# Performance work log

Hardware: AMD Instinct MI355X
Metric: run time of the kernel (lower is better)

## Reference

```python
import jax, jax.numpy as jnp
import numpy as np
from jax import lax

K = 5          # CARAFE kernel_size
S = 2          # scale_factor (downsample stride)
GROUP = 1      # mask groups
ENC_PAD = 1    # (encoder_kernel-1)*dilation//2 with encoder_kernel=3


def _conv2d(x, w, b, stride, padding, dilation=1):
    y = lax.conv_general_dilated(
        x, w, window_strides=(stride, stride),
        padding=[(padding, padding), (padding, padding)],
        rhs_dilation=(dilation, dilation),
        dimension_numbers=('NCHW', 'OIHW', 'NCHW'))
    return y + b[None, :, None, None]


def setup_inputs() -> dict:
    key = jax.random.key(0)
    k1, k2, k3 = jax.random.split(key, 3)
    B, C, H, W = 4, 256, 128, 128
    COMP = 64
    x = jax.random.normal(k1, (B, C, H, W), dtype=jnp.float32)
    # xavier-uniform-ish scale for compressor, std=0.001 for content encoder (as in init_weights)
    w1 = jax.random.normal(k2, (COMP, C, 1, 1), dtype=jnp.float32) * (1.0 / np.sqrt(C))
    b1 = jnp.zeros((COMP,), dtype=jnp.float32)
    w2 = jax.random.normal(k3, (K * K * GROUP, COMP, 3, 3), dtype=jnp.float32) * 0.001
    b2 = jnp.zeros((K * K * GROUP,), dtype=jnp.float32)
    return {"x": x, "w1": w1, "b1": b1, "w2": w2, "b2": b2}


def _carafe_forward(x, w1, b1, w2, b2):
    B, C, H, W = x.shape
    compressed = _conv2d(x, w1, b1, stride=1, padding=0)           # (B, 64, H, W)
    mask = _conv2d(compressed, w2, b2, stride=S, padding=ENC_PAD)   # (B, K*K*G, Ho, Wo)
    Ho, Wo = mask.shape[2], mask.shape[3]
    # kernel_normalizer: softmax over the K*K window per group
    mask = jax.nn.softmax(mask.reshape(B, GROUP, K * K, Ho, Wo), axis=2)
    # feature_reassemble: fused unfold * mask sum — accumulate per kernel tap to
    # avoid materializing the full (B, C, K*K, Ho, Wo) tensor.
    pad = K // 2
    x_pad = jnp.pad(x, ((0, 0), (0, 0), (pad, pad), (pad, pad)))
    Cg = C // GROUP
    out = jnp.zeros((B, GROUP, Cg, Ho, Wo), dtype=x.dtype)
    for i in range(K):
        for j in range(K):
            patch = x_pad[:, :, i:i + S * (Ho - 1) + 1:S, j:j + S * (Wo - 1) + 1:S]
            patch = patch.reshape(B, GROUP, Cg, Ho, Wo)
            out = out + patch * mask[:, :, i * K + j][:, :, None]
    return out.reshape(B, C, Ho, Wo)


def reference(x, w1, b1, w2, b2):
    return _carafe_forward(x, w1, b1, w2, b2)
```

## Files before the change

kernel.cpp:

```cpp
#include <hip/hip_runtime.h>
#include <math.h>

#define BN   4
#define CN   256
#define HN   128
#define WN   128
#define COMP 64
#define KK   25
#define HO   64
#define WO   64

#define W1B_OFF  0
#define W2A_OFF  8192
#define MASK_OFF 17408
#define COMP_OFF 427008
#define WS_NEED  ((size_t)(COMP_OFF + (size_t)BN * HN * WN * COMP / 2) * 4)

typedef short v8s  __attribute__((ext_vector_type(8)));
typedef float v16f __attribute__((ext_vector_type(16)));

__device__ inline ushort f2bf(float f) {
  unsigned u = __float_as_uint(f);
  return (ushort)((u + 0x7fffu + ((u >> 16) & 1u)) >> 16);
}

__global__ __launch_bounds__(64) void compose_frags(
    const float* __restrict__ w1, const float* __restrict__ w2,
    float* __restrict__ ws) {
  const int bid = blockIdx.x;
  const int lane = threadIdx.x;
  const int k0 = (lane >> 5) * 8;
  ushort pk[8];
  ushort* dst;
  if (bid < 32) {
    const int kidx = bid >> 1, nt = bid & 1;
    const int ch = nt * 32 + (lane & 31);
    const int c0 = kidx * 16 + k0;
#pragma unroll
    for (int j = 0; j < 8; ++j) pk[j] = f2bf(w1[(size_t)ch * CN + c0 + j]);
    dst = (ushort*)(ws + W1B_OFF) + ((size_t)((kidx * 2 + nt) * 64 + lane)) * 8;
  } else {
    const int g = bid - 32;
    const int t = g >> 2, kidx = g & 3;
    const int m = lane & 31;
    const int kk0 = kidx * 16 + k0;
#pragma unroll
    for (int j = 0; j < 8; ++j) {
      float v = (m < KK) ? w2[((size_t)(m * COMP + kk0 + j)) * 9 + t] : 0.f;
      pk[j] = f2bf(v);
    }
    dst = (ushort*)(ws + W2A_OFF) + ((size_t)((t * 4 + kidx) * 64 + lane)) * 8;
  }
  *(ushort4*)(dst)     = make_ushort4(pk[0], pk[1], pk[2], pk[3]);
  *(ushort4*)(dst + 4) = make_ushort4(pk[4], pk[5], pk[6], pk[7]);
}

__global__ __launch_bounds__(256, 4) void compress_kernel(
    const float* __restrict__ x, const float* __restrict__ b1,
    float* __restrict__ ws) {
  const int h = blockIdx.x, b = blockIdx.y;
  const int tid = threadIdx.x;
  const int lane = tid & 63, w = tid >> 6;
  const int nn = lane & 31, kh = lane >> 5;
  const int px = w * 32 + nn;
  const ushort* w1B = (const ushort*)(ws + W1B_OFF);
  v16f acc[2] = {{}, {}};
#pragma unroll 2
  for (int kidx = 0; kidx < 16; ++kidx) {
    const float* xc = x + (((size_t)(b * CN + kidx * 16 + kh * 8)) * HN + h) * WN + px;
    float av[8];
#pragma unroll
    for (int j = 0; j < 8; ++j) av[j] = xc[(size_t)j * (HN * WN)];
    v8s af;
#pragma unroll
    for (int j = 0; j < 8; ++j) af[j] = (short)f2bf(av[j]);
    v8s bf0 = *(const v8s*)(w1B + ((size_t)((kidx * 2 + 0) * 64 + lane)) * 8);
    v8s bf1 = *(const v8s*)(w1B + ((size_t)((kidx * 2 + 1) * 64 + lane)) * 8);
    acc[0] = __builtin_amdgcn_mfma_f32_32x32x16_bf16(af, bf0, acc[0], 0, 0, 0);
    acc[1] = __builtin_amdgcn_mfma_f32_32x32x16_bf16(af, bf1, acc[1], 0, 0, 0);
  }
  ushort* comp = (ushort*)(ws + COMP_OFF);
  const size_t rowbase = (size_t)(b * HN + h) * WN;
#pragma unroll
  for (int nt = 0; nt < 2; ++nt) {
    const float bias = b1[nt * 32 + nn];
#pragma unroll
    for (int rg = 0; rg < 16; ++rg) {
      const int pr = w * 32 + (rg & 3) + 8 * (rg >> 2) + 4 * kh;
      comp[(rowbase + pr) * COMP + nt * 32 + nn] = f2bf(acc[nt][rg] + bias);
    }
  }
}

#define MS_LDS 49152
__global__ __launch_bounds__(256, 4) void mask_softmax(
    const float* __restrict__ b2, float* __restrict__ ws) {
  const int ho = blockIdx.x, b = blockIdx.y;
  const int tid = threadIdx.x;
  const int lane = tid & 63, w = tid >> 6;
  __shared__ __attribute__((aligned(16))) char smem[MS_LDS];
  float* red = (float*)smem;
  const ushort* comp = (const ushort*)(ws + COMP_OFF);

#pragma unroll
  for (int i = 0; i < 12; ++i) {
    const int flat = i * 256 + tid;
    const int r = flat >> 10;
    const int px = (flat >> 3) & 127;
    const int cg = flat & 7;
    const int rr = 2 * ho + r - 1;
    v8s v = {};
    if (rr >= 0)
      v = *(const v8s*)(comp + ((size_t)(b * HN + rr) * WN + px) * COMP + cg * 8);
    const int boff = (((r * 128 + px) * 64 + cg * 8) * 2) ^ (((px >> 1) & 7) << 4);
    *(v8s*)(smem + boff) = v;
  }
  __syncthreads();

  const int nt = w & 1, kh2 = w >> 1;
  const int nn = lane & 31;
  const ushort* w2A = (const ushort*)(ws + W2A_OFF);
  const v8s zero8 = {};
  v16f acc = {};
#pragma unroll
  for (int t = 0; t < 9; ++t) {
    const int dr = t / 3, dc = t % 3;
#pragma unroll
    for (int ki = 0; ki < 2; ++ki) {
      const int kidx = kh2 * 2 + ki;
      const v8s af = *(const v8s*)(w2A + ((size_t)((t * 4 + kidx) * 64 + lane)) * 8);
      const int q = 2 * (nt * 32 + nn) + dc - 1;
      const bool bad = q < 0;
      const int qc = bad ? 0 : q;
      const int boff = (((dr * 128 + qc) * 64 + kidx * 16 + (lane >> 5) * 8) * 2)
                       ^ (((qc >> 1) & 7) << 4);
      v8s bf = *(const v8s*)(smem + boff);
      if (dc == 0 && bad) bf = zero8;
      acc = __builtin_amdgcn_mfma_f32_32x32x16_bf16(af, bf, acc, 0, 0, 0);
    }
  }
  __syncthreads();

  if (kh2 == 1) {
#pragma unroll
    for (int rg = 0; rg < 16; ++rg) {
      const int m = (rg & 3) + 8 * (rg >> 2) + 4 * (lane >> 5);
      if (m < KK) red[(nt * KK + m) * 32 + nn] = acc[rg];
    }
  }
  __syncthreads();
  if (kh2 == 0) {
#pragma unroll
    for (int rg = 0; rg < 16; ++rg) {
      const int m = (rg & 3) + 8 * (rg >> 2) + 4 * (lane >> 5);
      if (m < KK) red[(nt * KK + m) * 32 + nn] += acc[rg];
    }
  }
  __syncthreads();

  if (tid < 64) {
    const int wo = tid;
    const int tnt = wo >> 5, tc = wo & 31;
    float logit[KK];
    float mx = -1e30f;
#pragma unroll
    for (int m = 0; m < KK; ++m) {
      float l = b2[m] + red[(tnt * KK + m) * 32 + tc];
      logit[m] = l;
      mx = fmaxf(mx, l);
    }
    float ssum = 0.f;
#pragma unroll
    for (int m = 0; m < KK; ++m) {
      float e = __expf(logit[m] - mx);
      logit[m] = e;
      ssum += e;
    }
    const float inv = 1.f / ssum;
    float* mdst = ws + MASK_OFF + (size_t)(b * HO + ho) * KK * 64;
#pragma unroll
    for (int m = 0; m < KK; ++m) mdst[m * 64 + wo] = logit[m] * inv;
  }
}

__global__ __launch_bounds__(256, 4) void gather_kernel(
    const float* __restrict__ ws, const float* __restrict__ x,
    float* __restrict__ out) {
  const int bid0 = blockIdx.x;
  const int bid = (bid0 & 7) * 128 + (bid0 >> 3);
  const int ho = bid & 63;
  const int cq = (bid >> 6) & 3;
  const int b = bid >> 8;
  const int tid = threadIdx.x;
  const int lane = tid & 63, wv = tid >> 6;

  __shared__ float sml[KK * 64];

  const float* __restrict__ xb = x + (size_t)(b * CN) * (HN * WN);
  const int wo = lane;
  const int c_base = __builtin_amdgcn_readfirstlane(cq * 64 + wv * 16);
  const int col = 2 * wo;
  float2 g[2][5];
  auto load_g = [&](int ci, float2* dst) {
    const float* xc = xb + (size_t)(c_base + ci) * (HN * WN);
#pragma unroll
    for (int i = 0; i < 5; ++i) {
      int r = 2 * ho - 2 + i;
      dst[i] = (r >= 0 && r < HN) ? *(const float2*)(xc + r * WN + col)
                                  : make_float2(0.f, 0.f);
    }
  };
  load_g(0, g[0]);
  load_g(1, g[1]);

  const float* msrc = ws + MASK_OFF + (size_t)(b * HO + ho) * KK * 64;
  for (int i = tid; i < KK * 64; i += 256) sml[i] = msrc[i];
  __syncthreads();

  float smr[KK];
#pragma unroll
  for (int m = 0; m < KK; ++m) smr[m] = sml[m * 64 + wo];

  const float wok = (wo > 0) ? 1.f : 0.f;
  const float w63 = (wo < 63) ? 1.f : 0.f;
  for (int ci = 0; ci < 16; ++ci) {
    float2 v[5];
#pragma unroll
    for (int i = 0; i < 5; ++i) v[i] = g[ci & 1][i];
    if (ci + 2 < 16) load_g(ci + 2, g[ci & 1]);

    float acc2 = 0.f;
#pragma unroll
    for (int i = 0; i < 5; ++i) {
      float lx = wok * __shfl_up(v[i].x, 1, 64);
      float ly = wok * __shfl_up(v[i].y, 1, 64);
      float rx = w63 * __shfl_down(v[i].x, 1, 64);
      acc2 += lx * smr[i * 5 + 0] + ly * smr[i * 5 + 1]
            + v[i].x * smr[i * 5 + 2] + v[i].y * smr[i * 5 + 3]
            + rx * smr[i * 5 + 4];
    }
    out[(((size_t)(b * CN + c_base + ci)) * HO + ho) * WO + wo] = acc2;
  }
}

#define FB_WSTRIDE 240
#define FB_TB_OFF  (256 * FB_WSTRIDE)

__global__ __launch_bounds__(256) void compose_w_fb(
    const float* __restrict__ w1, const float* __restrict__ b1,
    const float* __restrict__ w2, float* __restrict__ ws) {
  int mt = blockIdx.x, c = threadIdx.x;
  float acc = 0.f;
#pragma unroll 8
  for (int k = 0; k < COMP; ++k)
    acc += w2[(size_t)(mt / 9 * COMP + k) * 9 + (mt % 9)] * w1[k * CN + c];
  ws[c * FB_WSTRIDE + mt] = acc;
  if (mt < FB_WSTRIDE - 225) ws[c * FB_WSTRIDE + 225 + mt] = 0.f;
  if (c == 0) {
    float tbv = 0.f;
    for (int k = 0; k < COMP; ++k)
      tbv += w2[(size_t)(mt / 9 * COMP + k) * 9 + (mt % 9)] * b1[k];
    ws[FB_TB_OFF + mt] = tbv;
  }
}

__global__ __launch_bounds__(1024, 4) void fused_fb(
    const float* __restrict__ x, const float* __restrict__ b2,
    const float* __restrict__ ws, float* __restrict__ out) {
  const int ho = blockIdx.x, b = blockIdx.y, tid = threadIdx.x;
  const int wo = tid & 63, wv = tid >> 6;
  const int c_base = __builtin_amdgcn_readfirstlane(wv * 16);
  const float* __restrict__ w2c = ws;
  const float* __restrict__ tb  = ws + FB_TB_OFF;
  __shared__ float red[8 * KK * 64];
  __shared__ float sm[KK * 64];
  const float* __restrict__ xb = x + (size_t)(b * CN) * (HN * WN);
  const int col = 2 * wo;
  float acc[KK];
#pragma unroll
  for (int m = 0; m < KK; ++m) acc[m] = 0.f;
  float2 xbuf[2][3];
  auto load_ch = [&](int ci, float2* dst) {
    const float* xc = xb + (size_t)(c_base + ci) * (HN * WN);
    dst[0] = (ho > 0) ? *(const float2*)(xc + (2 * ho - 1) * WN + col)
                      : make_float2(0.f, 0.f);
    dst[1] = *(const float2*)(xc + (2 * ho) * WN + col);
    dst[2] = *(const float2*)(xc + (2 * ho + 1) * WN + col);
  };
  load_ch(0, xbuf[0]);
  load_ch(1, xbuf[1]);
  const float wok = (wo > 0) ? 1.f : 0.f;
  for (int ci = 0; ci < 16; ++ci) {
    float2 r0 = xbuf[ci & 1][0], r1 = xbuf[ci & 1][1], r2 = xbuf[ci & 1][2];
    if (ci + 2 < 16) load_ch(ci + 2, xbuf[ci & 1]);
    float xv[9];
    xv[0] = wok * __shfl_up(r0.y, 1, 64); xv[1] = r0.x; xv[2] = r0.y;
    xv[3] = wok * __shfl_up(r1.y, 1, 64); xv[4] = r1.x; xv[5] = r1.y;
    xv[6] = wok * __shfl_up(r2.y, 1, 64); xv[7] = r2.x; xv[8] = r2.y;
    const float* __restrict__ wrow = w2c + (size_t)(c_base + ci) * FB_WSTRIDE;
#pragma unroll
    for (int m = 0; m < KK; ++m) {
      float a = acc[m];
#pragma unroll
      for (int t = 0; t < 9; ++t) a += wrow[m * 9 + t] * xv[t];
      acc[m] = a;
    }
  }
  float2 g[2][5];
  auto load_g = [&](int ci, float2* dst) {
    const float* xc = xb + (size_t)(c_base + ci) * (HN * WN);
#pragma unroll
    for (int i = 0; i < 5; ++i) {
      int r = 2 * ho - 2 + i;
      dst[i] = (r >= 0 && r < HN) ? *(const float2*)(xc + r * WN + col)
                                  : make_float2(0.f, 0.f);
    }
  };
  load_g(0, g[0]);
  load_g(1, g[1]);
  if (wv >= 8) {
#pragma unroll
    for (int m = 0; m < KK; ++m) red[((wv - 8) * KK + m) * 64 + wo] = acc[m];
  }
  __syncthreads();
  if (wv < 8) {
#pragma unroll
    for (int m = 0; m < KK; ++m) red[(wv * KK + m) * 64 + wo] += acc[m];
  }
  __syncthreads();
  if (wv < 4) {
#pragma unroll
    for (int m = 0; m < KK; ++m)
      red[(wv * KK + m) * 64 + wo] += red[((wv + 4) * KK + m) * 64 + wo];
  }
  __syncthreads();
  if (wv < 2) {
#pragma unroll
    for (int m = 0; m < KK; ++m)
      red[(wv * KK + m) * 64 + wo] += red[((wv + 2) * KK + m) * 64 + wo];
  }
  __syncthreads();
  if (tid < 64) {
    const float vr0 = (ho > 0) ? 1.f : 0.f;
    const float vq0 = (wo > 0) ? 1.f : 0.f;
    float logit[KK];
    float mx = -1e30f;
#pragma unroll
    for (int m = 0; m < KK; ++m) {
      const float* t9 = tb + m * 9;
      float l = b2[m]
              + vr0 * (vq0 * t9[0] + t9[1] + t9[2])
              +       (vq0 * t9[3] + t9[4] + t9[5])
              +       (vq0 * t9[6] + t9[7] + t9[8]);
      l += red[(0 * KK + m) * 64 + wo] + red[(1 * KK + m) * 64 + wo];
      logit[m] = l;
      mx = fmaxf(mx, l);
    }
    float s = 0.f;
#pragma unroll
    for (int m = 0; m < KK; ++m) {
      float e = __expf(logit[m] - mx);
      logit[m] = e;
      s += e;
    }
    float inv = 1.f / s;
#pragma unroll
    for (int m = 0; m < KK; ++m) sm[m * 64 + wo] = logit[m] * inv;
  }
  __syncthreads();
  float smr[KK];
#pragma unroll
  for (int m = 0; m < KK; ++m) smr[m] = sm[m * 64 + wo];
  const float w63 = (wo < 63) ? 1.f : 0.f;
  for (int ci = 0; ci < 16; ++ci) {
    float2 v[5];
#pragma unroll
    for (int i = 0; i < 5; ++i) v[i] = g[ci & 1][i];
    if (ci + 2 < 16) load_g(ci + 2, g[ci & 1]);
    float acc2 = 0.f;
#pragma unroll
    for (int i = 0; i < 5; ++i) {
      float lx = wok * __shfl_up(v[i].x, 1, 64);
      float ly = wok * __shfl_up(v[i].y, 1, 64);
      float rx = w63 * __shfl_down(v[i].x, 1, 64);
      acc2 += lx * smr[i * 5 + 0] + ly * smr[i * 5 + 1]
            + v[i].x * smr[i * 5 + 2] + v[i].y * smr[i * 5 + 3]
            + rx * smr[i * 5 + 4];
    }
    out[(((size_t)(b * CN + c_base + ci)) * HO + ho) * WO + wo] = acc2;
  }
}

extern "C" void kernel_launch(void* const* d_in, const int* in_sizes, int n_in,
                              void* d_out, int out_size, void* d_ws, size_t ws_size,
                              hipStream_t stream) {
  const float* x  = (const float*)d_in[0];
  const float* w1 = (const float*)d_in[1];
  const float* b1 = (const float*)d_in[2];
  const float* w2 = (const float*)d_in[3];
  const float* b2 = (const float*)d_in[4];
  float* out = (float*)d_out;
  float* ws  = (float*)d_ws;

  if (ws_size >= WS_NEED) {
    hipLaunchKernelGGL(compose_frags, dim3(68), dim3(64), 0, stream,
                       w1, w2, ws);
    hipLaunchKernelGGL(compress_kernel, dim3(HN, BN), dim3(256), 0, stream,
                       x, b1, ws);
    hipLaunchKernelGGL(mask_softmax, dim3(HO, BN), dim3(256), 0, stream,
                       b2, ws);
    hipLaunchKernelGGL(gather_kernel, dim3(1024), dim3(256), 0, stream,
                       ws, x, out);
  } else {
    hipLaunchKernelGGL(compose_w_fb, dim3(225), dim3(256), 0, stream,
                       w1, b1, w2, ws);
    hipLaunchKernelGGL(fused_fb, dim3(HO, BN), dim3(1024), 0, stream,
                       x, b2, ws, out);
  }
}
```

Before: 147.6 us.

## Fuse mask softmax into gather kernel, recomputing mask per channel half

Result: slower. 151.1 us (+2.3%).

```diff
diff --git a/kernel.cpp b/kernel.cpp
--- a/kernel.cpp
+++ b/kernel.cpp
@@ -92,19 +92,24 @@
   }
 }
 
-#define MS_LDS 49152
-__global__ __launch_bounds__(256, 4) void mask_softmax(
-    const float* __restrict__ b2, float* __restrict__ ws) {
-  const int ho = blockIdx.x, b = blockIdx.y;
+#define MG_SML 49152
+#define MG_LDS (49152 + 6400)
+__global__ __launch_bounds__(512, 4) void mask_gather(
+    const float* __restrict__ ws, const float* __restrict__ b2,
+    const float* __restrict__ x, float* __restrict__ out) {
+  const int ho = blockIdx.x, b = blockIdx.y, h = blockIdx.z;
   const int tid = threadIdx.x;
-  const int lane = tid & 63, w = tid >> 6;
-  __shared__ __attribute__((aligned(16))) char smem[MS_LDS];
+  const int lane = tid & 63, wv = tid >> 6;
+
+  __shared__ __attribute__((aligned(16))) char smem[MG_LDS];
   float* red = (float*)smem;
+  float* sml = (float*)(smem + MG_SML);
   const ushort* comp = (const ushort*)(ws + COMP_OFF);
-
-#pragma unroll
-  for (int i = 0; i < 12; ++i) {
-    const int flat = i * 256 + tid;
+  const float* __restrict__ xb = x + (size_t)(b * CN) * (HN * WN);
+
+#pragma unroll
+  for (int i = 0; i < 6; ++i) {
+    const int flat = i * 512 + tid;
     const int r = flat >> 10;
     const int px = (flat >> 3) & 127;
     const int cg = flat & 7;
@@ -117,28 +122,47 @@
   }
   __syncthreads();
 
-  const int nt = w & 1, kh2 = w >> 1;
+  const int nt = wv & 1, kh2 = wv >> 1;
   const int nn = lane & 31;
-  const ushort* w2A = (const ushort*)(ws + W2A_OFF);
-  const v8s zero8 = {};
   v16f acc = {};
-#pragma unroll
-  for (int t = 0; t < 9; ++t) {
-    const int dr = t / 3, dc = t % 3;
-#pragma unroll
-    for (int ki = 0; ki < 2; ++ki) {
-      const int kidx = kh2 * 2 + ki;
-      const v8s af = *(const v8s*)(w2A + ((size_t)((t * 4 + kidx) * 64 + lane)) * 8);
-      const int q = 2 * (nt * 32 + nn) + dc - 1;
-      const bool bad = q < 0;
-      const int qc = bad ? 0 : q;
-      const int boff = (((dr * 128 + qc) * 64 + kidx * 16 + (lane >> 5) * 8) * 2)
-                       ^ (((qc >> 1) & 7) << 4);
-      v8s bf = *(const v8s*)(smem + boff);
-      if (dc == 0 && bad) bf = zero8;
-      acc = __builtin_amdgcn_mfma_f32_32x32x16_bf16(af, bf, acc, 0, 0, 0);
-    }
-  }
+  if (wv < 4) {
+    const ushort* w2A = (const ushort*)(ws + W2A_OFF);
+    const v8s zero8 = {};
+#pragma unroll
+    for (int t = 0; t < 9; ++t) {
+      const int dr = t / 3, dc = t % 3;
+#pragma unroll
+      for (int ki = 0; ki < 2; ++ki) {
+        const int kidx = kh2 * 2 + ki;
+        const v8s af = *(const v8s*)(w2A + ((size_t)((t * 4 + kidx) * 64 + lane)) * 8);
+        const int q = 2 * (nt * 32 + nn) + dc - 1;
+        const bool bad = q < 0;
+        const int qc = bad ? 0 : q;
+        const int boff = (((dr * 128 + qc) * 64 + kidx * 16 + (lane >> 5) * 8) * 2)
+                         ^ (((qc >> 1) & 7) << 4);
+        v8s bf = *(const v8s*)(smem + boff);
+        if (dc == 0 && bad) bf = zero8;
+        acc = __builtin_amdgcn_mfma_f32_32x32x16_bf16(af, bf, acc, 0, 0, 0);
+      }
+    }
+  }
+
+  const int wo = lane;
+  const int c_base = __builtin_amdgcn_readfirstlane(h * 128 + wv * 16);
+  const int col = 2 * wo;
+  float2 g[2][5];
+  auto load_g = [&](int ci, float2* dst) {
+    const float* xc = xb + (size_t)(c_base + ci) * (HN * WN);
+#pragma unroll
+    for (int i = 0; i < 5; ++i) {
+      int r = 2 * ho - 2 + i;
+      dst[i] = (r >= 0 && r < HN) ? *(const float2*)(xc + r * WN + col)
+                                  : make_float2(0.f, 0.f);
+    }
+  };
+  load_g(0, g[0]);
+  load_g(1, g[1]);
+
   __syncthreads();
 
   if (kh2 == 1) {
@@ -159,8 +183,7 @@
   __syncthreads();
 
   if (tid < 64) {
-    const int wo = tid;
-    const int tnt = wo >> 5, tc = wo & 31;
+    const int tnt = tid >> 5, tc = tid & 31;
     float logit[KK];
     float mx = -1e30f;
 #pragma unroll
@@ -177,44 +200,9 @@
       ssum += e;
     }
     const float inv = 1.f / ssum;
-    float* mdst = ws + MASK_OFF + (size_t)(b * HO + ho) * KK * 64;
-#pragma unroll
-    for (int m = 0; m < KK; ++m) mdst[m * 64 + wo] = logit[m] * inv;
-  }
-}
-
-__global__ __launch_bounds__(256, 4) void gather_kernel(
-    const float* __restrict__ ws, const float* __restrict__ x,
-    float* __restrict__ out) {
-  const int bid0 = blockIdx.x;
-  const int bid = (bid0 & 7) * 128 + (bid0 >> 3);
-  const int ho = bid & 63;
-  const int cq = (bid >> 6) & 3;
-  const int b = bid >> 8;
-  const int tid = threadIdx.x;
-  const int lane = tid & 63, wv = tid >> 6;
-
-  __shared__ float sml[KK * 64];
-
-  const float* __restrict__ xb = x + (size_t)(b * CN) * (HN * WN);
-  const int wo = lane;
-  const int c_base = __builtin_amdgcn_readfirstlane(cq * 64 + wv * 16);
-  const int col = 2 * wo;
-  float2 g[2][5];
-  auto load_g = [&](int ci, float2* dst) {
-    const float* xc = xb + (size_t)(c_base + ci) * (HN * WN);
-#pragma unroll
-    for (int i = 0; i < 5; ++i) {
-      int r = 2 * ho - 2 + i;
-      dst[i] = (r >= 0 && r < HN) ? *(const float2*)(xc + r * WN + col)
-                                  : make_float2(0.f, 0.f);
-    }
-  };
-  load_g(0, g[0]);
-  load_g(1, g[1]);
-
-  const float* msrc = ws + MASK_OFF + (size_t)(b * HO + ho) * KK * 64;
-  for (int i = tid; i < KK * 64; i += 256) sml[i] = msrc[i];
+#pragma unroll
+    for (int m = 0; m < KK; ++m) sml[m * 64 + tid] = logit[m] * inv;
+  }
   __syncthreads();
 
   float smr[KK];
@@ -407,10 +395,8 @@
                        w1, w2, ws);
     hipLaunchKernelGGL(compress_kernel, dim3(HN, BN), dim3(256), 0, stream,
                        x, b1, ws);
-    hipLaunchKernelGGL(mask_softmax, dim3(HO, BN), dim3(256), 0, stream,
-                       b2, ws);
-    hipLaunchKernelGGL(gather_kernel, dim3(1024), dim3(256), 0, stream,
-                       ws, x, out);
+    hipLaunchKernelGGL(mask_gather, dim3(HO, BN, 2), dim3(512), 0, stream,
+                       ws, b2, x, out);
   } else {
     hipLaunchKernelGGL(compose_w_fb, dim3(225), dim3(256), 0, stream,
                        w1, b1, w2, ws);
```
